# Kernel tuning notes

Measured on AMD Instinct MI355X. Metric: run time of the kernel, lower is better.

The kernel has to match this reference:

```python
import jax, jax.numpy as jnp
import numpy as np

B, S, E, H = 2, 2048, 1024, 16
D = E // H  # head_dim = 64


def setup_inputs() -> dict:
    key = jax.random.key(0)
    ks = jax.random.split(key, 6)
    sc = 1.0 / np.sqrt(D)
    return {
        "x": jax.random.normal(ks[0], (B, S, E), dtype=jnp.float32),
        "Wq": jax.random.normal(ks[1], (D, D), dtype=jnp.float32) * sc,
        "Wk": jax.random.normal(ks[2], (D, D), dtype=jnp.float32) * sc,
        "Wv": jax.random.normal(ks[3], (D, D), dtype=jnp.float32) * sc,
        "Wo": jax.random.normal(ks[4], (E, E), dtype=jnp.float32) * (1.0 / np.sqrt(E)),
        "bo": jnp.zeros((E,), dtype=jnp.float32),
    }


def reference(x, Wq, Wk, Wv, Wo, bo):
    b, s, e = x.shape
    # split into heads: (B, H, S, D)
    xh = x.reshape(b, s, H, D).transpose(0, 2, 1, 3)
    # per-head linear projections (weights SHARED across heads); torch Linear: x @ W^T
    q = jnp.einsum('bhsd,ed->bhse', xh, Wq)
    k = jnp.einsum('bhsd,ed->bhse', xh, Wk)
    v = jnp.einsum('bhsd,ed->bhse', xh, Wv)
    # full attention matrix (B, H, S, S) — faithful to the naive original
    energy = jnp.einsum('bhqd,bhkd->bhqk', q, k)
    attn = jax.nn.softmax(energy / jnp.sqrt(jnp.asarray(D, x.dtype)), axis=-1)
    out = jnp.einsum('bhqk,bhkd->bhqd', attn, v)
    out = out.transpose(0, 2, 1, 3).reshape(b, s, e)
    return out @ Wo.T + bo
```

## Files before the change

kernel.cpp:

```cpp
#include <hip/hip_runtime.h>
#include <hip/hip_bf16.h>

#define B 2
#define S 2048
#define E 1024
#define H 16
#define D 64

typedef unsigned short ushort_t;
typedef __attribute__((ext_vector_type(8))) short bf16x8;
typedef __attribute__((ext_vector_type(4))) float f32x4;
typedef __attribute__((ext_vector_type(16))) float f32x16;

static __device__ __forceinline__ ushort_t f2bf(float f) {
    union { float f; unsigned u; } v; v.f = f;
    unsigned r = v.u + 0x7fffu + ((v.u >> 16) & 1u);
    return (ushort_t)(r >> 16);
}

#define MFMA(a, b, c)   __builtin_amdgcn_mfma_f32_16x16x32_bf16((a), (b), (c), 0, 0, 0)
#define MFMA32(a, b, c) __builtin_amdgcn_mfma_f32_32x32x16_bf16((a), (b), (c), 0, 0, 0)
#define PACKBF(hi, lo) __builtin_amdgcn_perm((hi), (lo), 0x07060302u)

__global__ __launch_bounds__(256) void qkv_proj(
    const float* __restrict__ x,
    const float* __restrict__ Wq, const float* __restrict__ Wk, const float* __restrict__ Wv,
    const float* __restrict__ Wo,
    ushort_t* __restrict__ q, ushort_t* __restrict__ k, ushort_t* __restrict__ vT,
    ushort_t* __restrict__ wob)
{
    __shared__ ushort_t Xs[64][72];
    __shared__ ushort_t Wqs[64][72], Wks[64][72], Wvs[64][72];
    int t = threadIdx.x;
    int bh = blockIdx.y, b = bh >> 4, h = bh & 15;
    int s0 = blockIdx.x * 64;

    {
        int woid = blockIdx.y * 32 + blockIdx.x;
        int i = woid * 1024 + t * 4;
        float4 f = *(const float4*)(Wo + i);
        ushort4 u2; u2.x = f2bf(f.x); u2.y = f2bf(f.y); u2.z = f2bf(f.z); u2.w = f2bf(f.w);
        *(ushort4*)(wob + i) = u2;
    }
    {
        int i = t >> 2, d0 = (t & 3) * 16;
        const float* xp = x + ((size_t)(b * S + s0 + i)) * E + h * D + d0;
        #pragma unroll
        for (int c = 0; c < 16; c += 4) {
            float4 f = *(const float4*)(xp + c);
            Xs[i][d0 + c + 0] = f2bf(f.x); Xs[i][d0 + c + 1] = f2bf(f.y);
            Xs[i][d0 + c + 2] = f2bf(f.z); Xs[i][d0 + c + 3] = f2bf(f.w);
        }
    }
    {
        int e = t >> 2, d0 = (t & 3) * 16;
        const float* wqp = Wq + e * 64 + d0;
        const float* wkp = Wk + e * 64 + d0;
        const float* wvp = Wv + e * 64 + d0;
        #pragma unroll
        for (int c = 0; c < 16; c += 4) {
            float4 fq = *(const float4*)(wqp + c);
            Wqs[e][d0 + c + 0] = f2bf(fq.x * 0.18033688011112042f);
            Wqs[e][d0 + c + 1] = f2bf(fq.y * 0.18033688011112042f);
            Wqs[e][d0 + c + 2] = f2bf(fq.z * 0.18033688011112042f);
            Wqs[e][d0 + c + 3] = f2bf(fq.w * 0.18033688011112042f);
            float4 fk = *(const float4*)(wkp + c);
            Wks[e][d0 + c + 0] = f2bf(fk.x); Wks[e][d0 + c + 1] = f2bf(fk.y);
            Wks[e][d0 + c + 2] = f2bf(fk.z); Wks[e][d0 + c + 3] = f2bf(fk.w);
            float4 fv = *(const float4*)(wvp + c);
            Wvs[e][d0 + c + 0] = f2bf(fv.x); Wvs[e][d0 + c + 1] = f2bf(fv.y);
            Wvs[e][d0 + c + 2] = f2bf(fv.z); Wvs[e][d0 + c + 3] = f2bf(fv.w);
        }
    }
    __syncthreads();

    int w = t >> 6, lane = t & 63, m = lane & 15, quad = lane >> 4;
    bf16x8 a0 = *(bf16x8*)&Xs[16 * w + m][quad * 8];
    bf16x8 a1 = *(bf16x8*)&Xs[16 * w + m][32 + quad * 8];
    f32x4 cq[4], ck[4], cv[4];
    #pragma unroll
    for (int nt = 0; nt < 4; nt++) { cq[nt] = (f32x4)0.f; ck[nt] = (f32x4)0.f; cv[nt] = (f32x4)0.f; }
    #pragma unroll
    for (int nt = 0; nt < 4; nt++) {
        bf16x8 b0, b1;
        b0 = *(bf16x8*)&Wqs[nt * 16 + m][quad * 8]; b1 = *(bf16x8*)&Wqs[nt * 16 + m][32 + quad * 8];
        cq[nt] = MFMA(a0, b0, cq[nt]); cq[nt] = MFMA(a1, b1, cq[nt]);
        b0 = *(bf16x8*)&Wks[nt * 16 + m][quad * 8]; b1 = *(bf16x8*)&Wks[nt * 16 + m][32 + quad * 8];
        ck[nt] = MFMA(a0, b0, ck[nt]); ck[nt] = MFMA(a1, b1, ck[nt]);
        b0 = *(bf16x8*)&Wvs[nt * 16 + m][quad * 8]; b1 = *(bf16x8*)&Wvs[nt * 16 + m][32 + quad * 8];
        cv[nt] = MFMA(a0, b0, cv[nt]); cv[nt] = MFMA(a1, b1, cv[nt]);
    }
    size_t base = (size_t)bh * S + s0;
    #pragma unroll
    for (int nt = 0; nt < 4; nt++)
        #pragma unroll
        for (int r = 0; r < 4; r++) {
            size_t idx = (base + 16 * w + quad * 4 + r) * D + nt * 16 + m;
            q[idx] = f2bf(cq[nt][r]);
            k[idx] = f2bf(ck[nt][r]);
        }
    __syncthreads();
    #pragma unroll
    for (int nt = 0; nt < 4; nt++)
        #pragma unroll
        for (int r = 0; r < 4; r++)
            Wvs[nt * 16 + m][16 * w + quad * 4 + r] = f2bf(cv[nt][r]);
    __syncthreads();
    {
        int d0 = t >> 2, sc = (t & 3) * 16;
        ushort_t* vp = vT + ((size_t)bh * D + d0) * S + s0 + sc;
        *(bf16x8*)(vp)     = *(bf16x8*)&Wvs[d0][sc];
        *(bf16x8*)(vp + 8) = *(bf16x8*)&Wvs[d0][sc + 8];
    }
}

__global__ __launch_bounds__(512, 4) void flash_attn(
    const ushort_t* __restrict__ q, const ushort_t* __restrict__ k,
    const ushort_t* __restrict__ vT, ushort_t* __restrict__ ao)
{
    __shared__ ushort_t Ks[2][2][64][72];
    __shared__ ushort_t Vt[2][2][64][72];
    int t = threadIdx.x;
    int bh = blockIdx.y, b = bh >> 4, h = bh & 15;
    int q0 = blockIdx.x * 128;
    int w = t >> 6, lane = t & 63, l31 = lane & 31, half = lane >> 5;
    int g = w >> 2, wq = w & 3;
    int tg = t & 255;

    const ushort_t* qb = q + ((size_t)bh * S + q0) * D;
    const ushort_t* kb = k + (size_t)bh * S * D;
    const ushort_t* vb = vT + (size_t)bh * D * S;

    bf16x8 qf[4];
    {
        const ushort_t* qp = qb + (size_t)(wq * 32 + l31) * D + half * 8;
        #pragma unroll
        for (int c = 0; c < 4; c++) qf[c] = *(const bf16x8*)(qp + c * 16);
    }

    f32x16 o0 = (f32x16)0.f, o1 = (f32x16)0.f;
    float2 ls2 = make_float2(0.f, 0.f);

    int sr = tg >> 2, scc = (tg & 3) * 16;
    bf16x8 kp0, kp1, vp0, vp1;

    {
        int k00 = g * 64;
        const ushort_t* kp = kb + (size_t)(k00 + sr) * D + scc;
        const ushort_t* vp = vb + (size_t)sr * S + k00 + scc;
        kp0 = *(const bf16x8*)(kp);     kp1 = *(const bf16x8*)(kp + 8);
        vp0 = *(const bf16x8*)(vp);     vp1 = *(const bf16x8*)(vp + 8);
        *(bf16x8*)&Ks[g][0][sr][scc]     = kp0;
        *(bf16x8*)&Ks[g][0][sr][scc + 8] = kp1;
        *(bf16x8*)&Vt[g][0][sr][scc]     = vp0;
        *(bf16x8*)&Vt[g][0][sr][scc + 8] = vp1;
    }
    __syncthreads();
    {
        int k01 = (2 + g) * 64;
        const ushort_t* kp = kb + (size_t)(k01 + sr) * D + scc;
        const ushort_t* vp = vb + (size_t)sr * S + k01 + scc;
        kp0 = *(const bf16x8*)(kp);     kp1 = *(const bf16x8*)(kp + 8);
        vp0 = *(const bf16x8*)(vp);     vp1 = *(const bf16x8*)(vp + 8);
    }

    const int NJ = S / 128;
    for (int jt = 0; jt < NJ; jt++) {
        int p = jt & 1;
        if (jt + 1 < NJ) {
            *(bf16x8*)&Ks[g][1 - p][sr][scc]     = kp0;
            *(bf16x8*)&Ks[g][1 - p][sr][scc + 8] = kp1;
            *(bf16x8*)&Vt[g][1 - p][sr][scc]     = vp0;
            *(bf16x8*)&Vt[g][1 - p][sr][scc + 8] = vp1;
        }
        if (jt + 2 < NJ) {
            int k0n = (2 * (jt + 2) + g) * 64;
            const ushort_t* kp = kb + (size_t)(k0n + sr) * D + scc;
            const ushort_t* vp = vb + (size_t)sr * S + k0n + scc;
            kp0 = *(const bf16x8*)(kp);     kp1 = *(const bf16x8*)(kp + 8);
            vp0 = *(const bf16x8*)(vp);     vp1 = *(const bf16x8*)(vp + 8);
        }

        union { unsigned u[4]; bf16x8 v; } pa[4];
        #pragma unroll
        for (int st = 0; st < 2; st++) {
            f32x16 e = (f32x16)0.f;
            #pragma unroll
            for (int c = 0; c < 4; c++) {
                bf16x8 ka = *(bf16x8*)&Ks[g][p][st * 32 + l31][c * 16 + half * 8];
                e = MFMA32(ka, qf[c], e);
            }
            unsigned pt[16];
            #pragma unroll
            for (int r = 0; r < 16; r += 2) {
                float pe0 = __builtin_amdgcn_exp2f(e[r]);
                float pe1 = __builtin_amdgcn_exp2f(e[r + 1]);
                ls2.x += pe0; ls2.y += pe1;
                pt[r]     = __float_as_uint(pe0);
                pt[r + 1] = __float_as_uint(pe1);
            }
            #pragma unroll
            for (int c2 = 0; c2 < 2; c2++) {
                int rb = c2 * 8;
                unsigned dA = PACKBF(pt[rb + 1], pt[rb + 0]);
                unsigned dB = PACKBF(pt[rb + 3], pt[rb + 2]);
                unsigned dC = PACKBF(pt[rb + 5], pt[rb + 4]);
                unsigned dD = PACKBF(pt[rb + 7], pt[rb + 6]);
                asm volatile("v_permlane32_swap_b32 %0, %1" : "+v"(dA), "+v"(dC));
                asm volatile("v_permlane32_swap_b32 %0, %1" : "+v"(dB), "+v"(dD));
                int kc = st * 2 + c2;
                pa[kc].u[0] = dA;
                pa[kc].u[1] = dB;
                pa[kc].u[2] = dC;
                pa[kc].u[3] = dD;
            }
        }

        #pragma unroll
        for (int kc = 0; kc < 4; kc++) {
            bf16x8 vf0 = *(bf16x8*)&Vt[g][p][l31][kc * 16 + half * 8];
            bf16x8 vf1 = *(bf16x8*)&Vt[g][p][32 + l31][kc * 16 + half * 8];
            o0 = MFMA32(pa[kc].v, vf0, o0);
            o1 = MFMA32(pa[kc].v, vf1, o1);
        }
        __syncthreads();
    }

    float lsum = ls2.x + ls2.y;
    float* cmb = (float*)&Ks[0][0][0][0];
    int slot = (wq * 64 + lane) * 33;
    if (g == 1) {
        #pragma unroll
        for (int r2 = 0; r2 < 16; r2++) { cmb[slot + r2] = o0[r2]; cmb[slot + 16 + r2] = o1[r2]; }
        cmb[slot + 32] = lsum;
    }
    __syncthreads();
    if (g == 0) {
        #pragma unroll
        for (int r2 = 0; r2 < 16; r2++) { o0[r2] += cmb[slot + r2]; o1[r2] += cmb[slot + 16 + r2]; }
        lsum += cmb[slot + 32];
        float lfull = lsum + __shfl_xor(lsum, 32, 64);
        float inv = 1.001953125f / lfull;
        #pragma unroll
        for (int reg = 0; reg < 16; reg++) {
            int qrow = (reg & 3) + 8 * (reg >> 2) + 4 * half;
            float li = __shfl(inv, qrow, 64);
            int srow = q0 + wq * 32 + qrow;
            size_t base2 = ((size_t)(b * S + srow)) * E + h * D + l31;
            ao[base2]      = f2bf(o0[reg] * li);
            ao[base2 + 32] = f2bf(o1[reg] * li);
        }
    }
}

__global__ __launch_bounds__(256) void out_proj(
    const ushort_t* __restrict__ A, const ushort_t* __restrict__ Wob,
    const float* __restrict__ bo, float* __restrict__ Y)
{
    __shared__ ushort_t As[2][128][72];
    __shared__ ushort_t Ws[2][64][72];
    int t = threadIdx.x;
    int hwb = blockIdx.y * 16 + blockIdx.x;
    int swz = (hwb & 7) * 64 + (hwb >> 3);
    int n0 = (swz & 15) * 64, m0 = (swz >> 4) * 128;
    int w = t >> 6, lane = t & 63, m = lane & 15, quad = lane >> 4;
    f32x4 acc[2][4];
    #pragma unroll
    for (int u = 0; u < 2; u++)
        #pragma unroll
        for (int nt = 0; nt < 4; nt++) acc[u][nt] = (f32x4)0.f;

    int ar = t >> 1, ac = (t & 1) * 32;
    int wr = t >> 2, wc = (t & 3) * 16;
    const ushort_t* apb = A + (size_t)(m0 + ar) * E + ac;
    const ushort_t* wpb = Wob + (size_t)(n0 + wr) * E + wc;

    bf16x8 arg[4], wrg[2];
    {
        #pragma unroll
        for (int i = 0; i < 4; i++) *(bf16x8*)&As[0][ar][ac + 8 * i] = *(const bf16x8*)(apb + 8 * i);
        *(bf16x8*)&Ws[0][wr][wc]     = *(const bf16x8*)(wpb);
        *(bf16x8*)&Ws[0][wr][wc + 8] = *(const bf16x8*)(wpb + 8);
    }
    __syncthreads();
    {
        #pragma unroll
        for (int i = 0; i < 4; i++) arg[i] = *(const bf16x8*)(apb + 64 + 8 * i);
        wrg[0] = *(const bf16x8*)(wpb + 64);
        wrg[1] = *(const bf16x8*)(wpb + 64 + 8);
    }

    const int KT = E / 64;
    for (int ks = 0; ks < KT; ks++) {
        int p = ks & 1;
        if (ks + 1 < KT) {
            #pragma unroll
            for (int i = 0; i < 4; i++) *(bf16x8*)&As[1 - p][ar][ac + 8 * i] = arg[i];
            *(bf16x8*)&Ws[1 - p][wr][wc]     = wrg[0];
            *(bf16x8*)&Ws[1 - p][wr][wc + 8] = wrg[1];
        }
        if (ks + 2 < KT) {
            int off = (ks + 2) * 64;
            #pragma unroll
            for (int i = 0; i < 4; i++) arg[i] = *(const bf16x8*)(apb + off + 8 * i);
            wrg[0] = *(const bf16x8*)(wpb + off);
            wrg[1] = *(const bf16x8*)(wpb + off + 8);
        }
        #pragma unroll
        for (int h2 = 0; h2 < 2; h2++) {
            bf16x8 af[2];
            af[0] = *(bf16x8*)&As[p][w * 32 + m][h2 * 32 + quad * 8];
            af[1] = *(bf16x8*)&As[p][w * 32 + 16 + m][h2 * 32 + quad * 8];
            #pragma unroll
            for (int nt = 0; nt < 4; nt++) {
                bf16x8 bfr = *(bf16x8*)&Ws[p][nt * 16 + m][h2 * 32 + quad * 8];
                acc[0][nt] = MFMA(af[0], bfr, acc[0][nt]);
                acc[1][nt] = MFMA(af[1], bfr, acc[1][nt]);
            }
        }
        __syncthreads();
    }
    #pragma unroll
    for (int u = 0; u < 2; u++)
        #pragma unroll
        for (int nt = 0; nt < 4; nt++)
            #pragma unroll
            for (int r = 0; r < 4; r++) {
                int row = m0 + w * 32 + u * 16 + quad * 4 + r;
                int col = n0 + nt * 16 + m;
                Y[(size_t)row * E + col] = acc[u][nt][r] + bo[col];
            }
}

extern "C" void kernel_launch(void* const* d_in, const int* in_sizes, int n_in,
                              void* d_out, int out_size, void* d_ws, size_t ws_size,
                              hipStream_t stream)
{
    const float* x  = (const float*)d_in[0];
    const float* Wq = (const float*)d_in[1];
    const float* Wk = (const float*)d_in[2];
    const float* Wv = (const float*)d_in[3];
    const float* Wo = (const float*)d_in[4];
    const float* bo = (const float*)d_in[5];
    float* Y = (float*)d_out;

    const size_t n = (size_t)B * H * S * D;
    ushort_t* qw  = (ushort_t*)d_ws;
    ushort_t* kw  = qw + n;
    ushort_t* vTw = kw + n;
    ushort_t* ao  = vTw + n;
    ushort_t* wob = ao + n;

    qkv_proj<<<dim3(S / 64, B * H), 256, 0, stream>>>(x, Wq, Wk, Wv, Wo, qw, kw, vTw, wob);
    flash_attn<<<dim3(S / 128, B * H), 512, 0, stream>>>(qw, kw, vTw, ao);
    out_proj<<<dim3(E / 64, (B * S) / 128), 256, 0, stream>>>(ao, wob, bo, Y);
}
```

Before: 147.9 us.

## Remap attention blocks per XCD, add MFMA priority hints, widen out_proj to 512 threads

The flash attention grid becomes 1D, and block indices are remapped so that each XCD (blockIdx mod 8) handles 4 whole (batch, head) pairs, keeping K/V reuse within one XCD's L2. s_setprio is raised around the QK and PV MFMA sequences so that waves issuing matrix ops get priority over waves doing softmax or loads. out_proj moves to 512 threads, with each wave computing a 16-row strip instead of 32 rows. That halves accumulator registers per wave and adds more waves to hide latency, at the cost of less B-fragment reuse per wave.

```diff
diff --git a/kernel.cpp b/kernel.cpp
--- a/kernel.cpp
+++ b/kernel.cpp
@@ -121,8 +121,11 @@
     __shared__ ushort_t Ks[2][2][64][72];
     __shared__ ushort_t Vt[2][2][64][72];
     int t = threadIdx.x;
-    int bh = blockIdx.y, b = bh >> 4, h = bh & 15;
-    int q0 = blockIdx.x * 128;
+    int lin = blockIdx.x;
+    int xcd = lin & 7, loc = lin >> 3;
+    int bh = xcd * 4 + (loc >> 4);
+    int q0 = (loc & 15) * 128;
+    int b = bh >> 4, h = bh & 15;
     int w = t >> 6, lane = t & 63, l31 = lane & 31, half = lane >> 5;
     int g = w >> 2, wq = w & 3;
     int tg = t & 255;
@@ -185,11 +188,13 @@
         #pragma unroll
         for (int st = 0; st < 2; st++) {
             f32x16 e = (f32x16)0.f;
+            __builtin_amdgcn_s_setprio(1);
             #pragma unroll
             for (int c = 0; c < 4; c++) {
                 bf16x8 ka = *(bf16x8*)&Ks[g][p][st * 32 + l31][c * 16 + half * 8];
                 e = MFMA32(ka, qf[c], e);
             }
+            __builtin_amdgcn_s_setprio(0);
             unsigned pt[16];
             #pragma unroll
             for (int r = 0; r < 16; r += 2) {
@@ -216,6 +221,7 @@
             }
         }
 
+        __builtin_amdgcn_s_setprio(1);
         #pragma unroll
         for (int kc = 0; kc < 4; kc++) {
             bf16x8 vf0 = *(bf16x8*)&Vt[g][p][l31][kc * 16 + half * 8];
@@ -223,6 +229,7 @@
             o0 = MFMA32(pa[kc].v, vf0, o0);
             o1 = MFMA32(pa[kc].v, vf1, o1);
         }
+        __builtin_amdgcn_s_setprio(0);
         __syncthreads();
     }
 
@@ -253,83 +260,72 @@
     }
 }
 
-__global__ __launch_bounds__(256) void out_proj(
+__global__ __launch_bounds__(512) void out_proj(
     const ushort_t* __restrict__ A, const ushort_t* __restrict__ Wob,
     const float* __restrict__ bo, float* __restrict__ Y)
 {
     __shared__ ushort_t As[2][128][72];
     __shared__ ushort_t Ws[2][64][72];
     int t = threadIdx.x;
-    int hwb = blockIdx.y * 16 + blockIdx.x;
+    int hwb = blockIdx.x;
     int swz = (hwb & 7) * 64 + (hwb >> 3);
     int n0 = (swz & 15) * 64, m0 = (swz >> 4) * 128;
     int w = t >> 6, lane = t & 63, m = lane & 15, quad = lane >> 4;
-    f32x4 acc[2][4];
-    #pragma unroll
-    for (int u = 0; u < 2; u++)
-        #pragma unroll
-        for (int nt = 0; nt < 4; nt++) acc[u][nt] = (f32x4)0.f;
-
-    int ar = t >> 1, ac = (t & 1) * 32;
-    int wr = t >> 2, wc = (t & 3) * 16;
+    f32x4 acc[4];
+    #pragma unroll
+    for (int nt = 0; nt < 4; nt++) acc[nt] = (f32x4)0.f;
+
+    int ar = t >> 2, ac = (t & 3) * 16;
+    int wr = t >> 3, wc = (t & 7) * 8;
     const ushort_t* apb = A + (size_t)(m0 + ar) * E + ac;
     const ushort_t* wpb = Wob + (size_t)(n0 + wr) * E + wc;
 
-    bf16x8 arg[4], wrg[2];
-    {
-        #pragma unroll
-        for (int i = 0; i < 4; i++) *(bf16x8*)&As[0][ar][ac + 8 * i] = *(const bf16x8*)(apb + 8 * i);
+    bf16x8 arg[2], wrg;
+    {
+        *(bf16x8*)&As[0][ar][ac]     = *(const bf16x8*)(apb);
+        *(bf16x8*)&As[0][ar][ac + 8] = *(const bf16x8*)(apb + 8);
         *(bf16x8*)&Ws[0][wr][wc]     = *(const bf16x8*)(wpb);
-        *(bf16x8*)&Ws[0][wr][wc + 8] = *(const bf16x8*)(wpb + 8);
-    }
-    __syncthreads();
-    {
-        #pragma unroll
-        for (int i = 0; i < 4; i++) arg[i] = *(const bf16x8*)(apb + 64 + 8 * i);
-        wrg[0] = *(const bf16x8*)(wpb + 64);
-        wrg[1] = *(const bf16x8*)(wpb + 64 + 8);
+    }
+    __syncthreads();
+    {
+        arg[0] = *(const bf16x8*)(apb + 64);
+        arg[1] = *(const bf16x8*)(apb + 64 + 8);
+        wrg    = *(const bf16x8*)(wpb + 64);
     }
 
     const int KT = E / 64;
     for (int ks = 0; ks < KT; ks++) {
         int p = ks & 1;
         if (ks + 1 < KT) {
-            #pragma unroll
-            for (int i = 0; i < 4; i++) *(bf16x8*)&As[1 - p][ar][ac + 8 * i] = arg[i];
-            *(bf16x8*)&Ws[1 - p][wr][wc]     = wrg[0];
-            *(bf16x8*)&Ws[1 - p][wr][wc + 8] = wrg[1];
+            *(bf16x8*)&As[1 - p][ar][ac]     = arg[0];
+            *(bf16x8*)&As[1 - p][ar][ac + 8] = arg[1];
+            *(bf16x8*)&Ws[1 - p][wr][wc]     = wrg;
         }
         if (ks + 2 < KT) {
             int off = (ks + 2) * 64;
-            #pragma unroll
-            for (int i = 0; i < 4; i++) arg[i] = *(const bf16x8*)(apb + off + 8 * i);
-            wrg[0] = *(const bf16x8*)(wpb + off);
-            wrg[1] = *(const bf16x8*)(wpb + off + 8);
+            arg[0] = *(const bf16x8*)(apb + off);
+            arg[1] = *(const bf16x8*)(apb + off + 8);
+            wrg    = *(const bf16x8*)(wpb + off);
         }
         #pragma unroll
         for (int h2 = 0; h2 < 2; h2++) {
-            bf16x8 af[2];
-            af[0] = *(bf16x8*)&As[p][w * 32 + m][h2 * 32 + quad * 8];
-            af[1] = *(bf16x8*)&As[p][w * 32 + 16 + m][h2 * 32 + quad * 8];
+            bf16x8 af = *(bf16x8*)&As[p][w * 16 + m][h2 * 32 + quad * 8];
             #pragma unroll
             for (int nt = 0; nt < 4; nt++) {
                 bf16x8 bfr = *(bf16x8*)&Ws[p][nt * 16 + m][h2 * 32 + quad * 8];
-                acc[0][nt] = MFMA(af[0], bfr, acc[0][nt]);
-                acc[1][nt] = MFMA(af[1], bfr, acc[1][nt]);
+                acc[nt] = MFMA(af, bfr, acc[nt]);
             }
         }
         __syncthreads();
     }
     #pragma unroll
-    for (int u = 0; u < 2; u++)
-        #pragma unroll
-        for (int nt = 0; nt < 4; nt++)
-            #pragma unroll
-            for (int r = 0; r < 4; r++) {
-                int row = m0 + w * 32 + u * 16 + quad * 4 + r;
-                int col = n0 + nt * 16 + m;
-                Y[(size_t)row * E + col] = acc[u][nt][r] + bo[col];
-            }
+    for (int nt = 0; nt < 4; nt++)
+        #pragma unroll
+        for (int r = 0; r < 4; r++) {
+            int row = m0 + w * 16 + quad * 4 + r;
+            int col = n0 + nt * 16 + m;
+            Y[(size_t)row * E + col] = acc[nt][r] + bo[col];
+        }
 }
 
 extern "C" void kernel_launch(void* const* d_in, const int* in_sizes, int n_in,
@@ -352,6 +348,6 @@
     ushort_t* wob = ao + n;
 
     qkv_proj<<<dim3(S / 64, B * H), 256, 0, stream>>>(x, Wq, Wk, Wv, Wo, qw, kw, vTw, wob);
-    flash_attn<<<dim3(S / 128, B * H), 512, 0, stream>>>(qw, kw, vTw, ao);
-    out_proj<<<dim3(E / 64, (B * S) / 128), 256, 0, stream>>>(ao, wob, bo, Y);
-}
+    flash_attn<<<dim3((S / 128) * B * H), 512, 0, stream>>>(qw, kw, vTw, ao);
+    out_proj<<<dim3(512), 512, 0, stream>>>(ao, wob, bo, Y);
+}
```

New measurement: 144.7 us. -2.2%, faster.
